# Kernel optimization log

Measured on AMD Instinct MI355X. Metric: run time of the kernel, lower is better.

Reference implementation:

```python
import jax, jax.numpy as jnp
import numpy as np

D = 128  # hidden_size

def setup_inputs() -> dict:
    key = jax.random.key(0)
    ks = jax.random.split(key, 10)
    N, K = 50000, 32
    x = jax.random.normal(ks[0], (N, D), dtype=jnp.float32)
    x_nb = jax.random.normal(ks[1], (N, K, D), dtype=jnp.float32)
    weight = jax.random.uniform(ks[2], (N, K), dtype=jnp.float32)
    s = 1.0 / np.sqrt(D)
    Wx = jax.random.uniform(ks[3], (D, D), jnp.float32, -s, s)
    bx = jax.random.uniform(ks[4], (D,), jnp.float32, -s, s)
    Wn = jax.random.uniform(ks[5], (D, D), jnp.float32, -s, s)
    bn = jax.random.uniform(ks[6], (D,), jnp.float32, -s, s)
    Ww = jax.random.uniform(ks[7], (D, 1), jnp.float32, -1.0, 1.0)
    bw = jax.random.uniform(ks[8], (D,), jnp.float32, -1.0, 1.0)
    Wl = jax.random.uniform(ks[9], (1, D), jnp.float32, -s, s)
    bl = jnp.zeros((1,), jnp.float32)
    return {"x": x, "x_nb": x_nb, "weight": weight,
            "Wx": Wx, "bx": bx, "Wn": Wn, "bn": bn,
            "Ww": Ww, "bw": bw, "Wl": Wl, "bl": bl}

def reference(x, x_nb, weight, Wx, bx, Wn, bn, Ww, bw, Wl, bl):
    # x: [N, d], x_nb: [N, K, d], weight: [N, K]
    x_s = x @ Wx.T + bx                      # [N, d]
    n_s = jnp.einsum('nkd,ed->nke', x_nb, Wn) + bn   # [N, K, d]
    w = weight[..., None] * Ww[:, 0] + bw    # [N, K, d] (Linear(1,d))
    h = x_s[:, None, :] + n_s + w            # [N, K, d]
    h = jnp.where(h >= 0, h, 0.1 * h)        # LeakyReLU(0.1)
    scores = jnp.einsum('nkd,d->nk', h, Wl[0]) + bl[0]  # [N, K]
    attn = jax.nn.softmax(scores, axis=1)    # softmax over neighbors
    out = jnp.einsum('nk,nkd->nd', attn, x_nb)
    return out
```

## Files before the change

### kernel.cpp

```cpp
#include <hip/hip_runtime.h>

#define D 128
#define KN 32

typedef __bf16 bf16x8 __attribute__((ext_vector_type(8)));
typedef float f32x4 __attribute__((ext_vector_type(4)));

__device__ __forceinline__ unsigned bfpack2(float a, float b) {
  unsigned ua = __float_as_uint(a), ub = __float_as_uint(b);
  ua += 0x7FFFu + ((ua >> 16) & 1u);
  ub += 0x7FFFu + ((ub >> 16) & 1u);
  return (ua >> 16) | (ub & 0xFFFF0000u);
}
__device__ __forceinline__ uint4 pack8(const float4& a, const float4& b) {
  uint4 r;
  r.x = bfpack2(a.x, a.y); r.y = bfpack2(a.z, a.w);
  r.z = bfpack2(b.x, b.y); r.w = bfpack2(b.z, b.w);
  return r;
}

__device__ __forceinline__ void lgkm_barrier() {
  __builtin_amdgcn_sched_barrier(0);
  asm volatile("s_waitcnt lgkmcnt(0)" ::: "memory");
  __builtin_amdgcn_s_barrier();
  __builtin_amdgcn_sched_barrier(0);
}


__device__ __forceinline__ void stage128_512(const float* __restrict__ src, int nrows,
                                             uint4* buf, int tid) {
  float4 v[4][2];
  #pragma unroll
  for (int i = 0; i < 4; ++i) {
    const int c = i * 512 + tid;
    const int row = c >> 4, slot = c & 15;
    if (row < nrows) {
      const float4* p = (const float4*)(src + (size_t)row * D + slot * 8);
      v[i][0] = p[0]; v[i][1] = p[1];
    } else {
      v[i][0] = make_float4(0.f, 0.f, 0.f, 0.f);
      v[i][1] = make_float4(0.f, 0.f, 0.f, 0.f);
    }
  }
  #pragma unroll
  for (int i = 0; i < 4; ++i) {
    const int c = i * 512 + tid;
    const int row = c >> 4, slot = c & 15;
    buf[row * 16 + (slot ^ (row & 7))] = pack8(v[i][0], v[i][1]);
  }
}

__device__ __forceinline__ void stage128_256(const float* __restrict__ src,
                                             uint4* buf, int tid) {
  #pragma unroll
  for (int i = 0; i < 8; ++i) {
    const int c = i * 256 + tid;
    const int row = c >> 4, slot = c & 15;
    const float4* p = (const float4*)(src + (size_t)row * D + slot * 8);
    buf[row * 16 + (slot ^ (row & 7))] = pack8(p[0], p[1]);
  }
}

__device__ __forceinline__ void stage64_load(const float* __restrict__ src, int tid,
                                             float4 v[4][2]) {
  #pragma unroll
  for (int i = 0; i < 4; ++i) {
    const int c = i * 256 + tid;
    const int row = c >> 4, slot = c & 15;
    const float4* p = (const float4*)(src + (size_t)row * D + slot * 8);
    v[i][0] = p[0]; v[i][1] = p[1];
  }
}
__device__ __forceinline__ void stage64_write(uint4* buf, int tid,
                                              const float4 v[4][2]) {
  #pragma unroll
  for (int i = 0; i < 4; ++i) {
    const int c = i * 256 + tid;
    const int row = c >> 4, slot = c & 15;
    buf[row * 16 + (slot ^ (row & 7))] = pack8(v[i][0], v[i][1]);
  }
}

__global__ __launch_bounds__(512, 4) void base_mfma(
    const float* __restrict__ x, const float* __restrict__ Wx,
    const float* __restrict__ bx, const float* __restrict__ bn,
    const float* __restrict__ bw, float* __restrict__ out, int N)
{
  __shared__ uint4 Bb[2048];
  __shared__ uint4 Ab[2048];
  __shared__ float bvec[D];
  const int tid = threadIdx.x;

  stage128_512(Wx, 128, Bb, tid);
  if (tid < D) bvec[tid] = bx[tid] + bn[tid] + bw[tid];

  const int lane = tid & 63, li = lane & 15, g = lane >> 4;
  const int wv = tid >> 6, rq = wv >> 1, ch = wv & 1;
  const int ntiles = (N + 127) >> 7;

  for (int t = blockIdx.x; t < ntiles; t += gridDim.x) {
    const int r0t = t << 7;
    __syncthreads();
    stage128_512(x + (size_t)r0t * D, N - r0t, Ab, tid);
    __syncthreads();

    f32x4 acc[2][4];
    #pragma unroll
    for (int i = 0; i < 2; ++i)
      #pragma unroll
      for (int j = 0; j < 4; ++j) acc[i][j] = (f32x4){0.f, 0.f, 0.f, 0.f};

    #pragma unroll
    for (int kb = 0; kb < 4; ++kb) {
      const int slot = kb * 4 + g;
      const int r0 = rq * 32 + li, r1 = r0 + 16;
      const bf16x8 a0 = __builtin_bit_cast(bf16x8, Ab[r0 * 16 + (slot ^ (r0 & 7))]);
      const bf16x8 a1 = __builtin_bit_cast(bf16x8, Ab[r1 * 16 + (slot ^ (r1 & 7))]);
      #pragma unroll
      for (int ct = 0; ct < 4; ++ct) {
        const int e = ch * 64 + ct * 16 + li;
        const bf16x8 b = __builtin_bit_cast(bf16x8, Bb[e * 16 + (slot ^ (e & 7))]);
        acc[0][ct] = __builtin_amdgcn_mfma_f32_16x16x32_bf16(a0, b, acc[0][ct], 0, 0, 0);
        acc[1][ct] = __builtin_amdgcn_mfma_f32_16x16x32_bf16(a1, b, acc[1][ct], 0, 0, 0);
      }
    }

    #pragma unroll
    for (int rt = 0; rt < 2; ++rt) {
      #pragma unroll
      for (int reg = 0; reg < 4; ++reg) {
        const int r = r0t + rq * 32 + rt * 16 + 4 * g + reg;
        if (r < N) {
          #pragma unroll
          for (int ct = 0; ct < 4; ++ct) {
            const int e = ch * 64 + ct * 16 + li;
            out[(size_t)r * D + e] = acc[rt][ct][reg] + bvec[e];
          }
        }
      }
    }
  }
}

__global__ __launch_bounds__(256, 3) void gnn_mfma(
    const float* __restrict__ x_nb, const float* __restrict__ weight,
    const float* __restrict__ Wn, const float* __restrict__ Ww,
    const float* __restrict__ Wl, float* __restrict__ out, int N)
{
  __shared__ uint4 Bb[2048];
  __shared__ uint4 Ab[1024];
  __shared__ float basel[2 * D];
  __shared__ float wwl[D], wll[D];
  __shared__ float wgt[2 * KN];
  __shared__ float spart[2][2][KN];
  __shared__ float attnl[2 * KN];
  const int tid = threadIdx.x;

  stage128_256(Wn, Bb, tid);
  if (tid < D) { wwl[tid] = Ww[tid]; wll[tid] = Wl[tid]; }

  const int lane = tid & 63, li = lane & 15, g = lane >> 4;
  const int wv = tid >> 6, rq = wv >> 1, ch = wv & 1;
  const int ntiles = N >> 1;

  float4 v[4][2];
  float basev = 0.f, wgtv = 0.f;

  int t = blockIdx.x;
  {
    stage64_load(x_nb + (size_t)(2 * t) * KN * D, tid, v);
    basev = out[(size_t)(2 * t) * D + tid];
    if (tid < 2 * KN) wgtv = weight[(size_t)(2 * t) * KN + tid];
    stage64_write(Ab, tid, v);
    basel[tid] = basev;
    if (tid < 2 * KN) wgt[tid] = wgtv;
  }
  __syncthreads();

  for (; t < ntiles; t += gridDim.x) {
    const int tn = t + gridDim.x;
    const bool have_next = (tn < ntiles);
    if (have_next) {
      stage64_load(x_nb + (size_t)(2 * tn) * KN * D, tid, v);
      basev = out[(size_t)(2 * tn) * D + tid];
      if (tid < 2 * KN) wgtv = weight[(size_t)(2 * tn) * KN + tid];
    }

    f32x4 acc[2][4];
    #pragma unroll
    for (int i = 0; i < 2; ++i)
      #pragma unroll
      for (int j = 0; j < 4; ++j) acc[i][j] = (f32x4){0.f, 0.f, 0.f, 0.f};

    #pragma unroll
    for (int kb = 0; kb < 4; ++kb) {
      const int slot = kb * 4 + g;
      const int r0 = rq * 32 + li, r1 = r0 + 16;
      const bf16x8 a0 = __builtin_bit_cast(bf16x8, Ab[r0 * 16 + (slot ^ (r0 & 7))]);
      const bf16x8 a1 = __builtin_bit_cast(bf16x8, Ab[r1 * 16 + (slot ^ (r1 & 7))]);
      #pragma unroll
      for (int ct = 0; ct < 4; ++ct) {
        const int e = ch * 64 + ct * 16 + li;
        const bf16x8 b = __builtin_bit_cast(bf16x8, Bb[e * 16 + (slot ^ (e & 7))]);
        acc[0][ct] = __builtin_amdgcn_mfma_f32_16x16x32_bf16(a0, b, acc[0][ct], 0, 0, 0);
        acc[1][ct] = __builtin_amdgcn_mfma_f32_16x16x32_bf16(a1, b, acc[1][ct], 0, 0, 0);
      }
    }

    float bvv[4], wwv[4], wlv[4];
    #pragma unroll
    for (int ct = 0; ct < 4; ++ct) {
      const int e = ch * 64 + ct * 16 + li;
      bvv[ct] = basel[rq * D + e];
      wwv[ct] = wwl[e];
      wlv[ct] = wll[e];
    }
    #pragma unroll
    for (int rt = 0; rt < 2; ++rt) {
      #pragma unroll
      for (int reg = 0; reg < 4; ++reg) {
        const int k = rt * 16 + 4 * g + reg;
        const float wk = wgt[rq * KN + k];
        float p = 0.f;
        #pragma unroll
        for (int ct = 0; ct < 4; ++ct) {
          float h = acc[rt][ct][reg] + bvv[ct] + wk * wwv[ct];
          h = fmaxf(h, 0.1f * h);
          p = fmaf(h, wlv[ct], p);
        }
        p += __shfl_xor(p, 1);
        p += __shfl_xor(p, 2);
        p += __shfl_xor(p, 4);
        p += __shfl_xor(p, 8);
        if (li == 0) spart[ch][rq][k] = p;
      }
    }
    lgkm_barrier();

    if (tid < 64) {
      const int node = tid >> 5, k = tid & 31;
      const float s = spart[0][node][k] + spart[1][node][k];
      float mx = s;
      #pragma unroll
      for (int m = 16; m >= 1; m >>= 1) mx = fmaxf(mx, __shfl_xor(mx, m));
      const float pe = __expf(s - mx);
      float sum = pe;
      #pragma unroll
      for (int m = 16; m >= 1; m >>= 1) sum += __shfl_xor(sum, m);
      attnl[node * KN + k] = pe / sum;
    }
    lgkm_barrier();

    if (wv < 2) {
      const int node = wv;
      const int slot = lane & 15, kg = lane >> 4;
      float p8[8];
      #pragma unroll
      for (int j = 0; j < 8; ++j) p8[j] = 0.f;
      #pragma unroll
      for (int kk = 0; kk < 8; ++kk) {
        const int k = kg * 8 + kk;
        const int row = node * KN + k;
        const uint4 u = Ab[row * 16 + (slot ^ kk)];
        const float a = attnl[node * KN + k];
        const unsigned uw[4] = {u.x, u.y, u.z, u.w};
        #pragma unroll
        for (int q = 0; q < 4; ++q) {
          p8[2 * q]     = fmaf(a, __uint_as_float(uw[q] << 16), p8[2 * q]);
          p8[2 * q + 1] = fmaf(a, __uint_as_float(uw[q] & 0xFFFF0000u), p8[2 * q + 1]);
        }
      }
      #pragma unroll
      for (int j = 0; j < 8; ++j) p8[j] += __shfl_xor(p8[j], 16);
      #pragma unroll
      for (int j = 0; j < 8; ++j) p8[j] += __shfl_xor(p8[j], 32);
      if (kg == 0) {
        float* o = out + (size_t)(2 * t + node) * D + slot * 8;
        *(float4*)(o)     = make_float4(p8[0], p8[1], p8[2], p8[3]);
        *(float4*)(o + 4) = make_float4(p8[4], p8[5], p8[6], p8[7]);
      }
    }
    lgkm_barrier();

    if (have_next) {
      stage64_write(Ab, tid, v);
      basel[tid] = basev;
      if (tid < 2 * KN) wgt[tid] = wgtv;
    }
    lgkm_barrier();
  }
}

extern "C" void kernel_launch(void* const* d_in, const int* in_sizes, int n_in,
                              void* d_out, int out_size, void* d_ws, size_t ws_size,
                              hipStream_t stream) {
  const float* x      = (const float*)d_in[0];
  const float* x_nb   = (const float*)d_in[1];
  const float* weight = (const float*)d_in[2];
  const float* Wx     = (const float*)d_in[3];
  const float* bx     = (const float*)d_in[4];
  const float* Wn     = (const float*)d_in[5];
  const float* bn     = (const float*)d_in[6];
  const float* Ww     = (const float*)d_in[7];
  const float* bw     = (const float*)d_in[8];
  const float* Wl     = (const float*)d_in[9];
  float* out = (float*)d_out;
  const int N = in_sizes[0] / D;

  base_mfma<<<dim3(391), dim3(512), 0, stream>>>(x, Wx, bx, bn, bw, out, N);
  gnn_mfma<<<dim3(768), dim3(256), 0, stream>>>(x_nb, weight, Wn, Ww, Wl, out, N);
}
```

Measured before the change: 201.7 us.

## Deepen register prefetch to two tiles ahead with ping-pong register buffers

Replaces the single-tile register prefetch with two register buffer sets (vA/vB), so global loads for the tile two iterations ahead are issued before computing the current tile. The loop is manually unrolled by two, and the loop body becomes a lambda. This aims to hide more HBM latency for the streaming x_nb reads, at the cost of doubling prefetch registers, which may lower occupancy or cause spills.

```diff
diff --git a/kernel.cpp b/kernel.cpp
--- a/kernel.cpp
+++ b/kernel.cpp
@@ -162,30 +162,12 @@
   const int lane = tid & 63, li = lane & 15, g = lane >> 4;
   const int wv = tid >> 6, rq = wv >> 1, ch = wv & 1;
   const int ntiles = N >> 1;
-
-  float4 v[4][2];
-  float basev = 0.f, wgtv = 0.f;
-
-  int t = blockIdx.x;
-  {
-    stage64_load(x_nb + (size_t)(2 * t) * KN * D, tid, v);
-    basev = out[(size_t)(2 * t) * D + tid];
-    if (tid < 2 * KN) wgtv = weight[(size_t)(2 * t) * KN + tid];
-    stage64_write(Ab, tid, v);
-    basel[tid] = basev;
-    if (tid < 2 * KN) wgt[tid] = wgtv;
-  }
-  __syncthreads();
-
-  for (; t < ntiles; t += gridDim.x) {
-    const int tn = t + gridDim.x;
-    const bool have_next = (tn < ntiles);
-    if (have_next) {
-      stage64_load(x_nb + (size_t)(2 * tn) * KN * D, tid, v);
-      basev = out[(size_t)(2 * tn) * D + tid];
-      if (tid < 2 * KN) wgtv = weight[(size_t)(2 * tn) * KN + tid];
-    }
-
+  const int gr = gridDim.x;
+
+  float4 vA[4][2], vB[4][2];
+  float basevA = 0.f, wgtvA = 0.f, basevB = 0.f, wgtvB = 0.f;
+
+  auto body = [&](int t) {
     f32x4 acc[2][4];
     #pragma unroll
     for (int i = 0; i < 2; ++i)
@@ -281,13 +263,59 @@
       }
     }
     lgkm_barrier();
-
-    if (have_next) {
-      stage64_write(Ab, tid, v);
-      basel[tid] = basev;
-      if (tid < 2 * KN) wgt[tid] = wgtv;
-    }
-    lgkm_barrier();
+  };
+
+  int t0 = blockIdx.x;
+  {
+    stage64_load(x_nb + (size_t)(2 * t0) * KN * D, tid, vA);
+    basevA = out[(size_t)(2 * t0) * D + tid];
+    if (tid < 2 * KN) wgtvA = weight[(size_t)(2 * t0) * KN + tid];
+    if (t0 + gr < ntiles) {
+      stage64_load(x_nb + (size_t)(2 * (t0 + gr)) * KN * D, tid, vB);
+      basevB = out[(size_t)(2 * (t0 + gr)) * D + tid];
+      if (tid < 2 * KN) wgtvB = weight[(size_t)(2 * (t0 + gr)) * KN + tid];
+    }
+    stage64_write(Ab, tid, vA);
+    basel[tid] = basevA;
+    if (tid < 2 * KN) wgt[tid] = wgtvA;
+  }
+  __syncthreads();
+
+  for (int t = t0; t < ntiles; t += 2 * gr) {
+    {
+      const int tis = t + 2 * gr;
+      if (tis < ntiles) {
+        stage64_load(x_nb + (size_t)(2 * tis) * KN * D, tid, vA);
+        basevA = out[(size_t)(2 * tis) * D + tid];
+        if (tid < 2 * KN) wgtvA = weight[(size_t)(2 * tis) * KN + tid];
+      }
+      body(t);
+      if (t + gr < ntiles) {
+        stage64_write(Ab, tid, vB);
+        basel[tid] = basevB;
+        if (tid < 2 * KN) wgt[tid] = wgtvB;
+      }
+      lgkm_barrier();
+    }
+    {
+      const int t2 = t + gr;
+      if (t2 < ntiles) {
+        const int tis = t + 3 * gr;
+        if (tis < ntiles) {
+          stage64_load(x_nb + (size_t)(2 * tis) * KN * D, tid, vB);
+          basevB = out[(size_t)(2 * tis) * D + tid];
+          if (tid < 2 * KN) wgtvB = weight[(size_t)(2 * tis) * KN + tid];
+        }
+        body(t2);
+        const int tc = t + 2 * gr;
+        if (tc < ntiles) {
+          stage64_write(Ab, tid, vA);
+          basel[tid] = basevA;
+          if (tid < 2 * KN) wgt[tid] = wgtvA;
+        }
+        lgkm_barrier();
+      }
+    }
   }
 }
 
```

New measurement: 356.9 us. 1.77x slower.

## Double-buffer neighbor tiles in LDS and prefetch two tiles ahead

Applied to the files above, without the earlier changes.

Splits the A-tile, base and weight LDS buffers into two halves so the next tile is written into the idle buffer at the start of each iteration while the current one is computed. Global loads are issued two tiles ahead, and one of the four barriers per iteration is removed. To fit the larger LDS footprint, occupancy drops from 3 to 2 blocks per CU and the grid shrinks from 768 to 512. The trade is fewer resident waves to hide memory latency against deeper software prefetch and less synchronisation.

```diff
diff --git a/kernel.cpp b/kernel.cpp
--- a/kernel.cpp
+++ b/kernel.cpp
@@ -142,16 +142,16 @@
   }
 }
 
-__global__ __launch_bounds__(256, 3) void gnn_mfma(
+__global__ __launch_bounds__(256, 2) void gnn_mfma(
     const float* __restrict__ x_nb, const float* __restrict__ weight,
     const float* __restrict__ Wn, const float* __restrict__ Ww,
     const float* __restrict__ Wl, float* __restrict__ out, int N)
 {
   __shared__ uint4 Bb[2048];
-  __shared__ uint4 Ab[1024];
-  __shared__ float basel[2 * D];
+  __shared__ uint4 Ab[2][1024];
+  __shared__ float basel[2][2 * D];
   __shared__ float wwl[D], wll[D];
-  __shared__ float wgt[2 * KN];
+  __shared__ float wgt[2][2 * KN];
   __shared__ float spart[2][2][KN];
   __shared__ float attnl[2 * KN];
   const int tid = threadIdx.x;
@@ -162,30 +162,41 @@
   const int lane = tid & 63, li = lane & 15, g = lane >> 4;
   const int wv = tid >> 6, rq = wv >> 1, ch = wv & 1;
   const int ntiles = N >> 1;
+  const int gr = gridDim.x;
 
   float4 v[4][2];
   float basev = 0.f, wgtv = 0.f;
 
-  int t = blockIdx.x;
+  const int t0 = blockIdx.x;
   {
-    stage64_load(x_nb + (size_t)(2 * t) * KN * D, tid, v);
-    basev = out[(size_t)(2 * t) * D + tid];
-    if (tid < 2 * KN) wgtv = weight[(size_t)(2 * t) * KN + tid];
-    stage64_write(Ab, tid, v);
-    basel[tid] = basev;
-    if (tid < 2 * KN) wgt[tid] = wgtv;
-  }
-  __syncthreads();
-
-  for (; t < ntiles; t += gridDim.x) {
-    const int tn = t + gridDim.x;
-    const bool have_next = (tn < ntiles);
-    if (have_next) {
-      stage64_load(x_nb + (size_t)(2 * tn) * KN * D, tid, v);
-      basev = out[(size_t)(2 * tn) * D + tid];
-      if (tid < 2 * KN) wgtv = weight[(size_t)(2 * tn) * KN + tid];
-    }
-
+    stage64_load(x_nb + (size_t)(2 * t0) * KN * D, tid, v);
+    basev = out[(size_t)(2 * t0) * D + tid];
+    if (tid < 2 * KN) wgtv = weight[(size_t)(2 * t0) * KN + tid];
+    stage64_write(Ab[0], tid, v);
+    basel[0][tid] = basev;
+    if (tid < 2 * KN) wgt[0][tid] = wgtv;
+    __syncthreads();
+    if (t0 + gr < ntiles) {
+      stage64_load(x_nb + (size_t)(2 * (t0 + gr)) * KN * D, tid, v);
+      basev = out[(size_t)(2 * (t0 + gr)) * D + tid];
+      if (tid < 2 * KN) wgtv = weight[(size_t)(2 * (t0 + gr)) * KN + tid];
+    }
+  }
+
+  int cur = 0;
+  for (int t = t0; t < ntiles; t += gr, cur ^= 1) {
+    if (t + gr < ntiles) {
+      stage64_write(Ab[1 - cur], tid, v);
+      basel[1 - cur][tid] = basev;
+      if (tid < 2 * KN) wgt[1 - cur][tid] = wgtv;
+      if (t + 2 * gr < ntiles) {
+        stage64_load(x_nb + (size_t)(2 * (t + 2 * gr)) * KN * D, tid, v);
+        basev = out[(size_t)(2 * (t + 2 * gr)) * D + tid];
+        if (tid < 2 * KN) wgtv = weight[(size_t)(2 * (t + 2 * gr)) * KN + tid];
+      }
+    }
+
+    const uint4* Abc = Ab[cur];
     f32x4 acc[2][4];
     #pragma unroll
     for (int i = 0; i < 2; ++i)
@@ -196,8 +207,8 @@
     for (int kb = 0; kb < 4; ++kb) {
       const int slot = kb * 4 + g;
       const int r0 = rq * 32 + li, r1 = r0 + 16;
-      const bf16x8 a0 = __builtin_bit_cast(bf16x8, Ab[r0 * 16 + (slot ^ (r0 & 7))]);
-      const bf16x8 a1 = __builtin_bit_cast(bf16x8, Ab[r1 * 16 + (slot ^ (r1 & 7))]);
+      const bf16x8 a0 = __builtin_bit_cast(bf16x8, Abc[r0 * 16 + (slot ^ (r0 & 7))]);
+      const bf16x8 a1 = __builtin_bit_cast(bf16x8, Abc[r1 * 16 + (slot ^ (r1 & 7))]);
       #pragma unroll
       for (int ct = 0; ct < 4; ++ct) {
         const int e = ch * 64 + ct * 16 + li;
@@ -211,7 +222,7 @@
     #pragma unroll
     for (int ct = 0; ct < 4; ++ct) {
       const int e = ch * 64 + ct * 16 + li;
-      bvv[ct] = basel[rq * D + e];
+      bvv[ct] = basel[cur][rq * D + e];
       wwv[ct] = wwl[e];
       wlv[ct] = wll[e];
     }
@@ -220,7 +231,7 @@
       #pragma unroll
       for (int reg = 0; reg < 4; ++reg) {
         const int k = rt * 16 + 4 * g + reg;
-        const float wk = wgt[rq * KN + k];
+        const float wk = wgt[cur][rq * KN + k];
         float p = 0.f;
         #pragma unroll
         for (int ct = 0; ct < 4; ++ct) {
@@ -261,7 +272,7 @@
       for (int kk = 0; kk < 8; ++kk) {
         const int k = kg * 8 + kk;
         const int row = node * KN + k;
-        const uint4 u = Ab[row * 16 + (slot ^ kk)];
+        const uint4 u = Abc[row * 16 + (slot ^ kk)];
         const float a = attnl[node * KN + k];
         const unsigned uw[4] = {u.x, u.y, u.z, u.w};
         #pragma unroll
@@ -279,13 +290,6 @@
         *(float4*)(o)     = make_float4(p8[0], p8[1], p8[2], p8[3]);
         *(float4*)(o + 4) = make_float4(p8[4], p8[5], p8[6], p8[7]);
       }
-    }
-    lgkm_barrier();
-
-    if (have_next) {
-      stage64_write(Ab, tid, v);
-      basel[tid] = basev;
-      if (tid < 2 * KN) wgt[tid] = wgtv;
     }
     lgkm_barrier();
   }
@@ -308,5 +312,5 @@
   const int N = in_sizes[0] / D;
 
   base_mfma<<<dim3(391), dim3(512), 0, stream>>>(x, Wx, bx, bn, bw, out, N);
-  gnn_mfma<<<dim3(768), dim3(256), 0, stream>>>(x_nb, weight, Wn, Ww, Wl, out, N);
-}
+  gnn_mfma<<<dim3(512), dim3(256), 0, stream>>>(x_nb, weight, Wn, Ww, Wl, out, N);
+}
```

Measured after the change: 216.4 us. +7.3%, slower.

## Reuse MFMA A-fragments in registers for attention-weighted sum across all waves

Applied to the files above, without the earlier changes.

The final attention-weighted neighbor sum now reuses the bf16 A-operand fragments already loaded into registers for the MFMA, spreading the work across all four waves instead of two, and reduces it with intra-row shuffles. The staging of the next tile into LDS moves to the top of the loop, which removes one barrier per iteration. This cuts LDS re-reads and barrier count. In exchange the kernel holds more registers live and issues more shuffles per output.

```diff
diff --git a/kernel.cpp b/kernel.cpp
--- a/kernel.cpp
+++ b/kernel.cpp
@@ -162,6 +162,7 @@
   const int lane = tid & 63, li = lane & 15, g = lane >> 4;
   const int wv = tid >> 6, rq = wv >> 1, ch = wv & 1;
   const int ntiles = N >> 1;
+  const int gr = gridDim.x;
 
   float4 v[4][2];
   float basev = 0.f, wgtv = 0.f;
@@ -171,21 +172,20 @@
     stage64_load(x_nb + (size_t)(2 * t) * KN * D, tid, v);
     basev = out[(size_t)(2 * t) * D + tid];
     if (tid < 2 * KN) wgtv = weight[(size_t)(2 * t) * KN + tid];
+  }
+
+  for (; t < ntiles; t += gr) {
     stage64_write(Ab, tid, v);
     basel[tid] = basev;
     if (tid < 2 * KN) wgt[tid] = wgtv;
-  }
-  __syncthreads();
-
-  for (; t < ntiles; t += gridDim.x) {
-    const int tn = t + gridDim.x;
-    const bool have_next = (tn < ntiles);
-    if (have_next) {
-      stage64_load(x_nb + (size_t)(2 * tn) * KN * D, tid, v);
-      basev = out[(size_t)(2 * tn) * D + tid];
-      if (tid < 2 * KN) wgtv = weight[(size_t)(2 * tn) * KN + tid];
-    }
-
+    if (t + gr < ntiles) {
+      stage64_load(x_nb + (size_t)(2 * (t + gr)) * KN * D, tid, v);
+      basev = out[(size_t)(2 * (t + gr)) * D + tid];
+      if (tid < 2 * KN) wgtv = weight[(size_t)(2 * (t + gr)) * KN + tid];
+    }
+    lgkm_barrier();
+
+    uint4 af[4][2];
     f32x4 acc[2][4];
     #pragma unroll
     for (int i = 0; i < 2; ++i)
@@ -196,8 +196,10 @@
     for (int kb = 0; kb < 4; ++kb) {
       const int slot = kb * 4 + g;
       const int r0 = rq * 32 + li, r1 = r0 + 16;
-      const bf16x8 a0 = __builtin_bit_cast(bf16x8, Ab[r0 * 16 + (slot ^ (r0 & 7))]);
-      const bf16x8 a1 = __builtin_bit_cast(bf16x8, Ab[r1 * 16 + (slot ^ (r1 & 7))]);
+      af[kb][0] = Ab[r0 * 16 + (slot ^ (r0 & 7))];
+      af[kb][1] = Ab[r1 * 16 + (slot ^ (r1 & 7))];
+      const bf16x8 a0 = __builtin_bit_cast(bf16x8, af[kb][0]);
+      const bf16x8 a1 = __builtin_bit_cast(bf16x8, af[kb][1]);
       #pragma unroll
       for (int ct = 0; ct < 4; ++ct) {
         const int e = ch * 64 + ct * 16 + li;
@@ -251,43 +253,36 @@
     }
     lgkm_barrier();
 
-    if (wv < 2) {
-      const int node = wv;
-      const int slot = lane & 15, kg = lane >> 4;
-      float p8[8];
-      #pragma unroll
-      for (int j = 0; j < 8; ++j) p8[j] = 0.f;
-      #pragma unroll
-      for (int kk = 0; kk < 8; ++kk) {
-        const int k = kg * 8 + kk;
-        const int row = node * KN + k;
-        const uint4 u = Ab[row * 16 + (slot ^ kk)];
-        const float a = attnl[node * KN + k];
-        const unsigned uw[4] = {u.x, u.y, u.z, u.w};
+    {
+      const float a0w = attnl[rq * KN + li];
+      const float a1w = attnl[rq * KN + li + 16];
+      #pragma unroll
+      for (int kbi = 0; kbi < 2; ++kbi) {
+        const int kb = 2 * ch + kbi;
+        const unsigned u0[4] = {af[kb][0].x, af[kb][0].y, af[kb][0].z, af[kb][0].w};
+        const unsigned u1[4] = {af[kb][1].x, af[kb][1].y, af[kb][1].z, af[kb][1].w};
+        float p[8];
         #pragma unroll
         for (int q = 0; q < 4; ++q) {
-          p8[2 * q]     = fmaf(a, __uint_as_float(uw[q] << 16), p8[2 * q]);
-          p8[2 * q + 1] = fmaf(a, __uint_as_float(uw[q] & 0xFFFF0000u), p8[2 * q + 1]);
-        }
-      }
-      #pragma unroll
-      for (int j = 0; j < 8; ++j) p8[j] += __shfl_xor(p8[j], 16);
-      #pragma unroll
-      for (int j = 0; j < 8; ++j) p8[j] += __shfl_xor(p8[j], 32);
-      if (kg == 0) {
-        float* o = out + (size_t)(2 * t + node) * D + slot * 8;
-        *(float4*)(o)     = make_float4(p8[0], p8[1], p8[2], p8[3]);
-        *(float4*)(o + 4) = make_float4(p8[4], p8[5], p8[6], p8[7]);
-      }
-    }
-    lgkm_barrier();
-
-    if (have_next) {
-      stage64_write(Ab, tid, v);
-      basel[tid] = basev;
-      if (tid < 2 * KN) wgt[tid] = wgtv;
-    }
-    lgkm_barrier();
+          p[2 * q] = a0w * __uint_as_float(u0[q] << 16)
+                   + a1w * __uint_as_float(u1[q] << 16);
+          p[2 * q + 1] = a0w * __uint_as_float(u0[q] & 0xFFFF0000u)
+                       + a1w * __uint_as_float(u1[q] & 0xFFFF0000u);
+        }
+        #pragma unroll
+        for (int j = 0; j < 8; ++j) {
+          p[j] += __shfl_xor(p[j], 1);
+          p[j] += __shfl_xor(p[j], 2);
+          p[j] += __shfl_xor(p[j], 4);
+          p[j] += __shfl_xor(p[j], 8);
+        }
+        if (li < 2) {
+          const int col = (kb * 4 + g) * 8 + li * 4;
+          *(float4*)(out + (size_t)(2 * t + rq) * D + col) =
+              make_float4(p[li * 4 + 0], p[li * 4 + 1], p[li * 4 + 2], p[li * 4 + 3]);
+        }
+      }
+    }
   }
 }
 
```

Result: slower. 397.4 us (+97.1%).
